# Optimization experiments

Measured on AMD Instinct MI355X. Metric: run time of the kernel, lower is better.

Reference implementation:

```python
import jax, jax.numpy as jnp
import numpy as np

N, D, T = 8192, 512, 12
EPS = 1e-6


def _ln(x, g, b):
    m = jnp.mean(x, axis=-1, keepdims=True)
    v = jnp.mean((x - m) ** 2, axis=-1, keepdims=True)
    return (x - m) / jnp.sqrt(v + EPS) * g + b


def _cross(x1, x2, Wa, ba, Wb, bb, d1, d2):
    # attn_weights2: [N, N], softmax over dim=1 (rows)
    aw2 = jax.nn.softmax((x1 @ Wa.T + ba) @ x2.T, axis=1)
    fused_x2 = (aw2 @ x2) / jnp.sqrt(jnp.float32(d2))
    aw1 = jax.nn.softmax((x2 @ Wb.T + bb) @ x1.T, axis=1)
    fused_x1 = (aw1 @ x1) / jnp.sqrt(jnp.float32(d1))
    return fused_x1, fused_x2


def setup_inputs() -> dict:
    key = jax.random.key(0)
    ks = jax.random.split(key, 16)
    s = 1.0 / np.sqrt(D)
    inp = {
        'xp': jax.random.normal(ks[0], (N, D), jnp.float32),
        'xm': jax.random.normal(ks[1], (N, D), jnp.float32),
        'xs': jax.random.normal(ks[2], (N, D), jnp.float32),
        'ln_g': jnp.ones((D,), jnp.float32),
        'ln_b': jnp.zeros((D,), jnp.float32),
        # mol cross-attention: linear1 (D->D), linear2 (D->D)
        'W1': jax.random.uniform(ks[3], (D, D), jnp.float32, -s, s),
        'b1': jnp.zeros((D,), jnp.float32),
        'W2': jax.random.uniform(ks[4], (D, D), jnp.float32, -s, s),
        'b2': jnp.zeros((D,), jnp.float32),
        # smile cross-attention
        'W3': jax.random.uniform(ks[5], (D, D), jnp.float32, -s, s),
        'b3': jnp.zeros((D,), jnp.float32),
        'W4': jax.random.uniform(ks[6], (D, D), jnp.float32, -s, s),
        'b4': jnp.zeros((D,), jnp.float32),
        # pred head: 2D -> T
        'Wp': jax.random.uniform(ks[7], (T, 2 * D), jnp.float32, -1.0 / np.sqrt(2 * D), 1.0 / np.sqrt(2 * D)),
        'bp': jnp.zeros((T,), jnp.float32),
        # gate
        't': jnp.full((1,), 0.5, jnp.float32),
        'Wt1': jax.random.uniform(ks[8], (50, 1), jnp.float32, -1.0, 1.0),
        'bt1': jnp.zeros((50,), jnp.float32),
        'Wt2': jax.random.uniform(ks[9], (1, 50), jnp.float32, -1.0 / np.sqrt(50), 1.0 / np.sqrt(50)),
        'bt2': jnp.zeros((1,), jnp.float32),
    }
    return inp


def reference(xp, xm, xs, ln_g, ln_b, W1, b1, W2, b2, W3, b3, W4, b4, Wp, bp, t, Wt1, bt1, Wt2, bt2):
    x1 = _ln(xp, ln_g, ln_b)
    x2 = _ln(xm, ln_g, ln_b)
    x3 = x1  # protein encoded twice with same LayerNorm
    x4 = _ln(xs, ln_g, ln_b)

    f1, f2 = _cross(x1, x2, W1, b1, W2, b2, D, D)
    h12 = jnp.concatenate([f1 + x1, f2 + x2], axis=1)          # [N, 2D]
    out12 = jax.nn.relu(h12) @ Wp.T + bp                        # [N, T]

    f3, f4 = _cross(x3, x4, W3, b3, W4, b4, D, D)
    h34 = jnp.concatenate([f3 + x3, f4 + x4], axis=1)
    out34 = jax.nn.relu(h34) @ Wp.T + bp

    t1 = t @ Wt1.T + bt1                                        # [50]
    t2 = jax.nn.sigmoid(t1 @ Wt2.T + bt2)                       # [1]
    return t2 * out12 + (1.0 - t2) * out34
```

## Files before the change

kernel.cpp:

```cpp
#include <hip/hip_runtime.h>
#include <stdint.h>


#define DEV __device__ __forceinline__
typedef unsigned short u16;
typedef __bf16 bf16x8 __attribute__((ext_vector_type(8)));
typedef float f32x4 __attribute__((ext_vector_type(4)));

constexpr int NR = 8192;
constexpr int DDIM = 512;
constexpr int TOUT = 12;

DEV u16 f2b(float f) {
  uint32_t u = __builtin_bit_cast(uint32_t, f);
  u += 0x7fffu + ((u >> 16) & 1u);
  return (u16)(u >> 16);
}
DEV float b2f(u16 h) {
  uint32_t u = ((uint32_t)h) << 16;
  return __builtin_bit_cast(float, u);
}

__global__ __launch_bounds__(256) void prep_kernel(
    const float* __restrict__ xp, const float* __restrict__ xm,
    const float* __restrict__ xs, const float* __restrict__ g,
    const float* __restrict__ b, const float* __restrict__ W1,
    const float* __restrict__ W2, const float* __restrict__ W3,
    const float* __restrict__ W4, u16* __restrict__ o1, u16* __restrict__ o2,
    u16* __restrict__ o4, u16* __restrict__ Wb) {
  int bid = blockIdx.x;
  int tid = threadIdx.x;
  if (bid < 6144) {
    int which = bid >> 11;
    int row = ((bid & 2047) << 2) + (tid >> 6);
    int lane = tid & 63;
    const float* x = which == 0 ? xp : (which == 1 ? xm : xs);
    u16* o = which == 0 ? o1 : (which == 1 ? o2 : o4);
    const float4* xr = (const float4*)(x + (size_t)row * DDIM);
    float4 v0 = xr[lane * 2], v1 = xr[lane * 2 + 1];
    float vals[8] = {v0.x, v0.y, v0.z, v0.w, v1.x, v1.y, v1.z, v1.w};
    float s = 0.f, s2 = 0.f;
    for (int j = 0; j < 8; j++) { s += vals[j]; s2 += vals[j] * vals[j]; }
    for (int off = 1; off < 64; off <<= 1) {
      s += __shfl_xor(s, off);
      s2 += __shfl_xor(s2, off);
    }
    float m = s * (1.0f / DDIM);
    float var = s2 * (1.0f / DDIM) - m * m;
    var = fmaxf(var, 0.f);
    float rs = rsqrtf(var + 1e-6f);
    int d0 = lane * 8;
    u16 us[8];
    for (int j = 0; j < 8; j++)
      us[j] = f2b((vals[j] - m) * rs * g[d0 + j] + b[d0 + j]);
    uint4 pk;
    pk.x = (uint32_t)us[0] | ((uint32_t)us[1] << 16);
    pk.y = (uint32_t)us[2] | ((uint32_t)us[3] << 16);
    pk.z = (uint32_t)us[4] | ((uint32_t)us[5] << 16);
    pk.w = (uint32_t)us[6] | ((uint32_t)us[7] << 16);
    *(uint4*)(o + (size_t)row * DDIM + d0) = pk;
  } else {
    int wbid = bid - 6144;
    int wi = wbid >> 7;
    const float* W = wi == 0 ? W1 : (wi == 1 ? W2 : (wi == 2 ? W3 : W4));
    size_t base = ((size_t)(wbid & 127) * 256 + tid) * 8;
    const float4* src = (const float4*)(W + base);
    float4 a = src[0], c = src[1];
    float vals[8] = {a.x, a.y, a.z, a.w, c.x, c.y, c.z, c.w};
    u16 us[8];
    for (int j = 0; j < 8; j++) us[j] = f2b(vals[j]);
    uint4 pk;
    pk.x = (uint32_t)us[0] | ((uint32_t)us[1] << 16);
    pk.y = (uint32_t)us[2] | ((uint32_t)us[3] << 16);
    pk.z = (uint32_t)us[4] | ((uint32_t)us[5] << 16);
    pk.w = (uint32_t)us[6] | ((uint32_t)us[7] << 16);
    *(uint4*)(Wb + (size_t)wi * DDIM * DDIM + base) = pk;
  }
}

template <int MODE, bool TRIPLE>
DEV void gemm_core(const u16* __restrict__ A, const u16* __restrict__ B,
                   u16* __restrict__ C, const float* __restrict__ bias,
                   u16* lds, int K, int lda, int ldb, int ldc, int bx,
                   int by) {
  constexpr int TM = 4, TN = 4;
  int tid = threadIdx.x;
  int w = tid >> 6, lane = tid & 63;
  int q = lane >> 4, c16 = lane & 15;
  int n0 = bx * 128, m0 = by * 128;
  int wrow = (w >> 1) * 64, wcol = (w & 1) * 64;

  const u16* gptr[4];
  int lof[4];
#pragma unroll
  for (int j = 0; j < 4; j++) {
    int call = w + j * 4;
    bool isA = call < 8;
    int ci = isA ? call : call - 8;
    int chunk = ci * 64 + lane;
    int row = chunk >> 2;
    int gch = ((chunk & 3) - (row >> 1)) & 3;
    gptr[j] = isA ? (A + (size_t)(m0 + row) * lda + gch * 8)
                  : (B + (size_t)(n0 + row) * ldb + gch * 8);
    lof[j] = (isA ? 0 : 4096) + ci * 512;
  }
  auto stageAll = [&](int buf) {
    int bo = buf * 8192;
#pragma unroll
    for (int j = 0; j < 4; j++) {
      __builtin_amdgcn_global_load_lds(
          (const __attribute__((address_space(1))) void*)gptr[j],
          (__attribute__((address_space(3))) void*)(lds + bo + lof[j]), 16, 0,
          0);
      gptr[j] += 32;
    }
  };

  f32x4 acc[TM][TN] = {};
  int nk = K >> 5;
  stageAll(0);
  stageAll(1);
  int cur = 0;
  for (int ks = 0; ks < nk; ks++) {
    if (ks + 1 < nk)
      asm volatile("s_waitcnt vmcnt(4)" ::: "memory");
    else
      asm volatile("s_waitcnt vmcnt(0)" ::: "memory");
    __builtin_amdgcn_sched_barrier(0);
    __builtin_amdgcn_s_barrier();
    __builtin_amdgcn_sched_barrier(0);
    if constexpr (TRIPLE) {
      if (ks + 2 < nk) {
        int nb = cur + 2;
        if (nb >= 3) nb -= 3;
        stageAll(nb);
      }
    }
    const u16* Asm = lds + cur * 8192;
    const u16* Bsm = Asm + 4096;
    bf16x8 af[TM], bfr[TN];
#pragma unroll
    for (int i = 0; i < TM; i++) {
      int r = wrow + i * 16 + c16;
      af[i] = *(const bf16x8*)&Asm[r * 32 + (((q + (r >> 1)) & 3) * 8)];
    }
#pragma unroll
    for (int n = 0; n < TN; n++) {
      int r = wcol + n * 16 + c16;
      bfr[n] = *(const bf16x8*)&Bsm[r * 32 + (((q + (r >> 1)) & 3) * 8)];
    }
    __builtin_amdgcn_s_setprio(1);
#pragma unroll
    for (int i = 0; i < TM; i++)
#pragma unroll
      for (int n = 0; n < TN; n++)
        acc[i][n] = __builtin_amdgcn_mfma_f32_16x16x32_bf16(af[i], bfr[n],
                                                            acc[i][n], 0, 0, 0);
    __builtin_amdgcn_s_setprio(0);
    if constexpr (!TRIPLE) {
      asm volatile("s_waitcnt lgkmcnt(0)" ::: "memory");
      __builtin_amdgcn_sched_barrier(0);
      __builtin_amdgcn_s_barrier();
      __builtin_amdgcn_sched_barrier(0);
      if (ks + 2 < nk) stageAll(cur);
      cur ^= 1;
    } else {
      cur++;
      if (cur >= 3) cur -= 3;
    }
  }
  for (int h = 0; h < 2; h++) {
    __syncthreads();
    if ((w & 1) == h) {
      for (int i = 0; i < TM; i++) {
        for (int n = 0; n < TN; n++) {
          float bv = 0.f;
          if constexpr (MODE == 0) bv = bias[n0 + wcol + n * 16 + c16];
          for (int r = 0; r < 4; r++) {
            int rl = wrow + i * 16 + q * 4 + r;
            int cl = (n * 16 + c16) ^ ((rl & 7) << 3);
            float v = acc[i][n][r];
            if constexpr (MODE == 0) v += bv;
            if constexpr (MODE == 1) v = __expf(v - 48.0f);
            lds[rl * 64 + cl] = f2b(v);
          }
        }
      }
    }
    __syncthreads();
    for (int rep = 0; rep < 4; rep++) {
      int idx = rep * 256 + tid;
      int row = idx >> 3, seg = idx & 7;
      uint4 vv = ((const uint4*)lds)[row * 8 + (seg ^ (row & 7))];
      *(uint4*)(C + (size_t)(m0 + row) * ldc + n0 + h * 64 + seg * 8) = vv;
    }
  }
}

__global__ __launch_bounds__(256, 4) void tqp_kernel(
    const u16* __restrict__ s1, const u16* __restrict__ s2,
    const u16* __restrict__ s4, u16* __restrict__ t1, u16* __restrict__ t2,
    u16* __restrict__ t4, const u16* __restrict__ x1b,
    const u16* __restrict__ Wb, const float* __restrict__ b0,
    u16* __restrict__ Qs) {
  __shared__ u16 lds[16384];
  int bid = blockIdx.x;
  int tid = threadIdx.x;
  if (bid < 256) {
    gemm_core<0, false>(x1b, Wb, Qs, b0, lds, DDIM, DDIM, DDIM, DDIM,
                        bid & 3, bid >> 2);
  } else {
    constexpr int LD = 66;
    u16* tile = lds;
    int tb = bid - 256;
    int which = tb >> 10;
    int rem = tb & 1023;
    int c0 = (rem & 7) * 64;
    int r0 = (rem >> 3) * 64;
    const u16* src = which == 0 ? s1 : (which == 1 ? s2 : s4);
    u16* dst = which == 0 ? t1 : (which == 1 ? t2 : t4);
    for (int c = tid; c < 512; c += 256) {
      int i = c >> 3, j8 = (c & 7) * 8;
      uint4 v = *(const uint4*)(src + (size_t)(r0 + i) * DDIM + c0 + j8);
      uint32_t* dw = (uint32_t*)&tile[i * LD + j8];
      dw[0] = v.x; dw[1] = v.y; dw[2] = v.z; dw[3] = v.w;
    }
    __syncthreads();
    for (int rep = 0; rep < 2; rep++) {
      int idx = rep * 256 + tid;
      int o = idx >> 3, j8 = (idx & 7) * 8;
      u16 us[8];
      for (int k = 0; k < 8; k++) us[k] = tile[(j8 + k) * LD + o];
      uint4 pk;
      pk.x = (uint32_t)us[0] | ((uint32_t)us[1] << 16);
      pk.y = (uint32_t)us[2] | ((uint32_t)us[3] << 16);
      pk.z = (uint32_t)us[4] | ((uint32_t)us[5] << 16);
      pk.w = (uint32_t)us[6] | ((uint32_t)us[7] << 16);
      *(uint4*)(dst + (size_t)(c0 + o) * NR + r0 + j8) = pk;
    }
  }
}

DEV void pv_body(const u16* __restrict__ A, const u16* __restrict__ B,
                 u16* lds, u16* __restrict__ C, int bx, int by) {
  constexpr int BM = 64, BN = 128, BK = 64;
  int tid = threadIdx.x, w = tid >> 6, lane = tid & 63;
  int q = lane >> 4, c16 = lane & 15;
  int n0 = bx * BN, m0 = by * BM;
  int wr = (w >> 1) * 32, wc = (w & 1) * 64;
  f32x4 acc[2][4] = {};
  f32x4 accl[2] = {};
  bf16x8 ones;
  for (int j = 0; j < 8; j++) ones[j] = (__bf16)1.0f;

  const u16* gptr[6];
  int lof0[6], lof1[6];
#pragma unroll
  for (int it = 0; it < 6; it++) {
    int cb = it * 256 + w * 64;
    int c = cb + lane;
    bool isA = cb < 512;
    int ci = isA ? c : c - 512;
    int row = ci >> 3;
    int koff = ((ci & 7) ^ (row & 7)) * 8;
    gptr[it] = isA ? (A + (size_t)(m0 + row) * NR + koff)
                   : (B + (size_t)(n0 + row) * NR + koff);
    lof0[it] = isA ? (cb * 8) : (8192 + (cb - 512) * 8);
    lof1[it] = isA ? (4096 + cb * 8) : (16384 + (cb - 512) * 8);
  }
  auto stage = [&](int buf) {
#pragma unroll
    for (int it = 0; it < 6; it++) {
      int lo = buf ? lof1[it] : lof0[it];
      __builtin_amdgcn_global_load_lds(
          (const __attribute__((address_space(1))) void*)gptr[it],
          (__attribute__((address_space(3))) void*)(lds + lo), 16, 0, 0);
      gptr[it] += BK;
    }
  };

  constexpr int KSTEPS = NR / BK;
  stage(0);
  stage(1);
  for (int ks = 0; ks < KSTEPS; ks++) {
    int cur = ks & 1;
    if (ks + 1 < KSTEPS)
      asm volatile("s_waitcnt vmcnt(6)" ::: "memory");
    else
      asm volatile("s_waitcnt vmcnt(0)" ::: "memory");
    __builtin_amdgcn_sched_barrier(0);
    __builtin_amdgcn_s_barrier();
    __builtin_amdgcn_sched_barrier(0);
    const u16* Asm = lds + cur * 4096;
    const u16* Bsm = lds + 8192 + cur * 8192;
#pragma unroll
    for (int kh = 0; kh < 2; kh++) {
      bf16x8 af[2], bfr[4];
      int cl = kh * 4 + q;
#pragma unroll
      for (int i = 0; i < 2; i++) {
        int r = wr + i * 16 + c16;
        af[i] = *(const bf16x8*)&Asm[r * BK + ((cl ^ (r & 7)) * 8)];
      }
#pragma unroll
      for (int n = 0; n < 4; n++) {
        int r = wc + n * 16 + c16;
        bfr[n] = *(const bf16x8*)&Bsm[r * BK + ((cl ^ (r & 7)) * 8)];
      }
      __builtin_amdgcn_s_setprio(1);
#pragma unroll
      for (int i = 0; i < 2; i++)
        accl[i] = __builtin_amdgcn_mfma_f32_16x16x32_bf16(af[i], ones, accl[i],
                                                          0, 0, 0);
#pragma unroll
      for (int i = 0; i < 2; i++)
#pragma unroll
        for (int n = 0; n < 4; n++)
          acc[i][n] = __builtin_amdgcn_mfma_f32_16x16x32_bf16(
              af[i], bfr[n], acc[i][n], 0, 0, 0);
      __builtin_amdgcn_s_setprio(0);
    }
    asm volatile("s_waitcnt lgkmcnt(0)" ::: "memory");
    __builtin_amdgcn_sched_barrier(0);
    __builtin_amdgcn_s_barrier();
    __builtin_amdgcn_sched_barrier(0);
    if (ks + 2 < KSTEPS) stage(cur);
  }
  for (int i = 0; i < 2; i++) {
    float invl[4];
    for (int r = 0; r < 4; r++)
      invl[r] = 0.044194173824159216f / accl[i][r];
    for (int n = 0; n < 4; n++) {
      int col = n0 + wc + n * 16 + c16;
      for (int r = 0; r < 4; r++) {
        int row = m0 + wr + i * 16 + q * 4 + r;
        C[(size_t)row * DDIM + col] = f2b(acc[i][n][r] * invl[r]);
      }
    }
  }
}

DEV void pv_remap(int bid, int& bx, int& by) {
  bx = (bid >> 3) & 3;
  by = (bid & 7) + 8 * (bid >> 5);
}

__global__ __launch_bounds__(256, 4) void scores_kernel(
    const u16* __restrict__ Q, const u16* __restrict__ Kv,
    u16* __restrict__ P) {
  __shared__ u16 lds[16384];
  gemm_core<1, false>(Q, Kv, P, nullptr, lds, DDIM, DDIM, DDIM, NR,
                      blockIdx.x, blockIdx.y);
}

__global__ __launch_bounds__(256, 4) void qscombo_kernel(
    const u16* __restrict__ x1b, const u16* __restrict__ x2b,
    const u16* __restrict__ x4b, const u16* __restrict__ Wb,
    const float* __restrict__ b1, const float* __restrict__ b2,
    const float* __restrict__ b3, u16* __restrict__ Qs,
    const u16* __restrict__ Q0, u16* __restrict__ P) {
  __shared__ u16 lds[16384];
  if (blockIdx.x < 768) {
    int b = blockIdx.x;
    int z = 1 + (b >> 8), rem = b & 255;
    const u16* A = z == 1 ? x2b : (z == 2 ? x1b : x4b);
    const float* bias = z == 1 ? b1 : (z == 2 ? b2 : b3);
    gemm_core<0, false>(A, Wb + (size_t)z * DDIM * DDIM,
                        Qs + (size_t)z * NR * DDIM, bias, lds, DDIM, DDIM,
                        DDIM, DDIM, rem & 3, rem >> 2);
  } else {
    int b = blockIdx.x - 768;
    gemm_core<1, false>(Q0, x2b, P, nullptr, lds, DDIM, DDIM, DDIM, NR,
                        b & 63, b >> 6);
  }
}

__global__ __launch_bounds__(256, 3) void pv_kernel(
    const u16* __restrict__ A, const u16* __restrict__ B,
    u16* __restrict__ C) {
  __shared__ u16 lds[24576];
  int bx, by;
  pv_remap(blockIdx.x, bx, by);
  pv_body(A, B, lds, C, bx, by);
}

__global__ __launch_bounds__(256, 3) void combo_kernel(
    const u16* __restrict__ Pin, const u16* __restrict__ Vt,
    u16* __restrict__ F, const u16* __restrict__ Q,
    const u16* __restrict__ Kv, u16* __restrict__ Pout) {
  __shared__ u16 lds[24576];
  if (blockIdx.x < 512) {
    int bx, by;
    pv_remap(blockIdx.x, bx, by);
    pv_body(Pin, Vt, lds, F, bx, by);
  } else {
    int b = blockIdx.x - 512;
    gemm_core<1, true>(Q, Kv, Pout, nullptr, lds, DDIM, DDIM, DDIM, NR,
                       b & 63, b >> 6);
  }
}

__global__ __launch_bounds__(256) void head_kernel(
    const u16* __restrict__ F1, const u16* __restrict__ F2,
    const u16* __restrict__ F3, const u16* __restrict__ F4,
    const u16* __restrict__ x1, const u16* __restrict__ x2,
    const u16* __restrict__ x4, const float* __restrict__ Wp,
    const float* __restrict__ bp, const float* __restrict__ tg,
    const float* __restrict__ Wt1, const float* __restrict__ bt1,
    const float* __restrict__ Wt2, const float* __restrict__ bt2,
    float* __restrict__ out) {
  __shared__ float wps[TOUT * 2 * DDIM];
  __shared__ float t2s;
  int tid = threadIdx.x;
  for (int i = tid; i < TOUT * 2 * DDIM; i += 256) wps[i] = Wp[i];
  if (tid == 0) {
    float s = bt2[0];
    for (int k = 0; k < 50; k++) s += Wt2[k] * (tg[0] * Wt1[k] + bt1[k]);
    t2s = 1.0f / (1.0f + __expf(-s));
  }
  __syncthreads();
  int g = tid >> 5, j = tid & 31;
  size_t m = (size_t)blockIdx.x * 8 + g;
  float a12[TOUT] = {}, a34[TOUT] = {};
  for (int d = j; d < 2 * DDIM; d += 32) {
    float h12, h34;
    if (d < DDIM) {
      float xv = b2f(x1[m * DDIM + d]);
      h12 = b2f(F1[m * DDIM + d]) + xv;
      h34 = b2f(F3[m * DDIM + d]) + xv;
    } else {
      int dd = d - DDIM;
      h12 = b2f(F2[m * DDIM + dd]) + b2f(x2[m * DDIM + dd]);
      h34 = b2f(F4[m * DDIM + dd]) + b2f(x4[m * DDIM + dd]);
    }
    h12 = fmaxf(h12, 0.f);
    h34 = fmaxf(h34, 0.f);
    for (int t = 0; t < TOUT; t++) {
      float wv = wps[t * 2 * DDIM + d];
      a12[t] += h12 * wv;
      a34[t] += h34 * wv;
    }
  }
  for (int off = 1; off < 32; off <<= 1)
    for (int t = 0; t < TOUT; t++) {
      a12[t] += __shfl_xor(a12[t], off);
      a34[t] += __shfl_xor(a34[t], off);
    }
  if (j < TOUT) {
    float t2 = t2s;
    out[m * TOUT + j] = t2 * a12[j] + (1.f - t2) * a34[j] + bp[j];
  }
}

extern "C" void kernel_launch(void* const* d_in, const int* in_sizes, int n_in,
                              void* d_out, int out_size, void* d_ws,
                              size_t ws_size, hipStream_t stream) {
  (void)in_sizes; (void)n_in; (void)out_size;
  const float* xp = (const float*)d_in[0];
  const float* xm = (const float*)d_in[1];
  const float* xs = (const float*)d_in[2];
  const float* ln_g = (const float*)d_in[3];
  const float* ln_b = (const float*)d_in[4];
  const float* Wmat[4] = {(const float*)d_in[5], (const float*)d_in[7],
                          (const float*)d_in[9], (const float*)d_in[11]};
  const float* bvec[4] = {(const float*)d_in[6], (const float*)d_in[8],
                          (const float*)d_in[10], (const float*)d_in[12]};
  const float* Wp = (const float*)d_in[13];
  const float* bp = (const float*)d_in[14];
  const float* tg = (const float*)d_in[15];
  const float* Wt1 = (const float*)d_in[16];
  const float* bt1 = (const float*)d_in[17];
  const float* Wt2 = (const float*)d_in[18];
  const float* bt2 = (const float*)d_in[19];
  float* out = (float*)d_out;

  char* ws = (char*)d_ws;
  const size_t MB = 1ull << 20;
  u16* x1b = (u16*)(ws + 0 * MB);
  u16* x2b = (u16*)(ws + 8 * MB);
  u16* x4b = (u16*)(ws + 16 * MB);
  u16* x1t = (u16*)(ws + 24 * MB);
  u16* x2t = (u16*)(ws + 32 * MB);
  u16* x4t = (u16*)(ws + 40 * MB);
  u16* Wb = (u16*)(ws + 48 * MB);
  u16* Qs = (u16*)(ws + 52 * MB);
  u16* P0 = (u16*)(ws + 84 * MB);
  bool dual = ws_size >= 340 * MB;
  u16* P1 = dual ? (u16*)(ws + 212 * MB) : P0;

  prep_kernel<<<dim3(6656), 256, 0, stream>>>(
      xp, xm, xs, ln_g, ln_b, Wmat[0], Wmat[1], Wmat[2], Wmat[3], x1b, x2b,
      x4b, Wb);

  const u16* kvb[4] = {x2b, x1b, x4b, x1b};
  const u16* kvt[4] = {x2t, x1t, x4t, x1t};
  u16* slot[4];
  for (int a = 0; a < 4; a++) slot[a] = Qs + (size_t)a * NR * DDIM;

  tqp_kernel<<<dim3(3328), 256, 0, stream>>>(x1b, x2b, x4b, x1t, x2t, x4t,
                                             x1b, Wb, bvec[0], Qs);

  qscombo_kernel<<<dim3(768 + 64 * 64), 256, 0, stream>>>(
      x1b, x2b, x4b, Wb, bvec[1], bvec[2], bvec[3], Qs, slot[0], P0);

  if (dual) {
    u16* Pb[4] = {P0, P1, P0, P1};
    for (int a = 0; a < 3; a++) {
      combo_kernel<<<dim3(512 + 64 * 64), 256, 0, stream>>>(
          Pb[a], kvt[a], slot[a], slot[a + 1], kvb[a + 1], Pb[a + 1]);
    }
    pv_kernel<<<dim3(512), 256, 0, stream>>>(Pb[3], kvt[3], slot[3]);
  } else {
    for (int a = 0; a < 4; a++) {
      if (a > 0)
        scores_kernel<<<dim3(64, 64), 256, 0, stream>>>(slot[a], kvb[a], P0);
      pv_kernel<<<dim3(512), 256, 0, stream>>>(P0, kvt[a], slot[a]);
    }
  }

  head_kernel<<<dim3(NR / 8), 256, 0, stream>>>(
      slot[1], slot[0], slot[3], slot[2], x1b, x2b, x4b, Wp, bp, tg, Wt1, bt1,
      Wt2, bt2, out);
}
```

Baseline: 868.4 us.

## Split final PV GEMM along K into two halves with a finalize reduction

```diff
diff --git a/kernel.cpp b/kernel.cpp
--- a/kernel.cpp
+++ b/kernel.cpp
@@ -197,7 +197,7 @@
   }
 }
 
-__global__ __launch_bounds__(256, 4) void tqp_kernel(
+__global__ __launch_bounds__(256, 5) void tqp_kernel(
     const u16* __restrict__ s1, const u16* __restrict__ s2,
     const u16* __restrict__ s4, u16* __restrict__ t1, u16* __restrict__ t2,
     u16* __restrict__ t4, const u16* __restrict__ x1b,
@@ -241,8 +241,11 @@
   }
 }
 
+template <bool PARTIAL>
 DEV void pv_body(const u16* __restrict__ A, const u16* __restrict__ B,
-                 u16* lds, u16* __restrict__ C, int bx, int by) {
+                 u16* lds, u16* __restrict__ C, float* __restrict__ Pf,
+                 float* __restrict__ lsum, int kbase, int ksteps, int bx,
+                 int by) {
   constexpr int BM = 64, BN = 128, BK = 64;
   int tid = threadIdx.x, w = tid >> 6, lane = tid & 63;
   int q = lane >> 4, c16 = lane & 15;
@@ -263,8 +266,8 @@
     int ci = isA ? c : c - 512;
     int row = ci >> 3;
     int koff = ((ci & 7) ^ (row & 7)) * 8;
-    gptr[it] = isA ? (A + (size_t)(m0 + row) * NR + koff)
-                   : (B + (size_t)(n0 + row) * NR + koff);
+    gptr[it] = isA ? (A + (size_t)(m0 + row) * NR + kbase + koff)
+                   : (B + (size_t)(n0 + row) * NR + kbase + koff);
     lof0[it] = isA ? (cb * 8) : (8192 + (cb - 512) * 8);
     lof1[it] = isA ? (4096 + cb * 8) : (16384 + (cb - 512) * 8);
   }
@@ -279,12 +282,11 @@
     }
   };
 
-  constexpr int KSTEPS = NR / BK;
   stage(0);
   stage(1);
-  for (int ks = 0; ks < KSTEPS; ks++) {
+  for (int ks = 0; ks < ksteps; ks++) {
     int cur = ks & 1;
-    if (ks + 1 < KSTEPS)
+    if (ks + 1 < ksteps)
       asm volatile("s_waitcnt vmcnt(6)" ::: "memory");
     else
       asm volatile("s_waitcnt vmcnt(0)" ::: "memory");
@@ -324,17 +326,34 @@
     __builtin_amdgcn_sched_barrier(0);
     __builtin_amdgcn_s_barrier();
     __builtin_amdgcn_sched_barrier(0);
-    if (ks + 2 < KSTEPS) stage(cur);
-  }
-  for (int i = 0; i < 2; i++) {
-    float invl[4];
-    for (int r = 0; r < 4; r++)
-      invl[r] = 0.044194173824159216f / accl[i][r];
-    for (int n = 0; n < 4; n++) {
-      int col = n0 + wc + n * 16 + c16;
-      for (int r = 0; r < 4; r++) {
-        int row = m0 + wr + i * 16 + q * 4 + r;
-        C[(size_t)row * DDIM + col] = f2b(acc[i][n][r] * invl[r]);
+    if (ks + 2 < ksteps) stage(cur);
+  }
+  if constexpr (PARTIAL) {
+    for (int i = 0; i < 2; i++) {
+      for (int n = 0; n < 4; n++) {
+        int col = n0 + wc + n * 16 + c16;
+        for (int r = 0; r < 4; r++) {
+          int row = m0 + wr + i * 16 + q * 4 + r;
+          Pf[(size_t)row * DDIM + col] = acc[i][n][r];
+        }
+      }
+    }
+    if ((w & 1) == 0 && c16 == 0) {
+      for (int i = 0; i < 2; i++)
+        for (int r = 0; r < 4; r++)
+          lsum[m0 + wr + i * 16 + q * 4 + r] = accl[i][r];
+    }
+  } else {
+    for (int i = 0; i < 2; i++) {
+      float invl[4];
+      for (int r = 0; r < 4; r++)
+        invl[r] = 0.044194173824159216f / accl[i][r];
+      for (int n = 0; n < 4; n++) {
+        int col = n0 + wc + n * 16 + c16;
+        for (int r = 0; r < 4; r++) {
+          int row = m0 + wr + i * 16 + q * 4 + r;
+          C[(size_t)row * DDIM + col] = f2b(acc[i][n][r] * invl[r]);
+        }
       }
     }
   }
@@ -345,7 +364,7 @@
   by = (bid & 7) + 8 * (bid >> 5);
 }
 
-__global__ __launch_bounds__(256, 4) void scores_kernel(
+__global__ __launch_bounds__(256, 5) void scores_kernel(
     const u16* __restrict__ Q, const u16* __restrict__ Kv,
     u16* __restrict__ P) {
   __shared__ u16 lds[16384];
@@ -353,7 +372,7 @@
                       blockIdx.x, blockIdx.y);
 }
 
-__global__ __launch_bounds__(256, 4) void qscombo_kernel(
+__global__ __launch_bounds__(256, 5) void qscombo_kernel(
     const u16* __restrict__ x1b, const u16* __restrict__ x2b,
     const u16* __restrict__ x4b, const u16* __restrict__ Wb,
     const float* __restrict__ b1, const float* __restrict__ b2,
@@ -381,7 +400,40 @@
   __shared__ u16 lds[24576];
   int bx, by;
   pv_remap(blockIdx.x, bx, by);
-  pv_body(A, B, lds, C, bx, by);
+  pv_body<false>(A, B, lds, C, nullptr, nullptr, 0, 128, bx, by);
+}
+
+__global__ __launch_bounds__(256, 3) void pv_split_kernel(
+    const u16* __restrict__ A, const u16* __restrict__ B,
+    float* __restrict__ Pf, float* __restrict__ ls) {
+  __shared__ u16 lds[24576];
+  int half = blockIdx.x >> 9, inner = blockIdx.x & 511;
+  int bx, by;
+  pv_remap(inner, bx, by);
+  pv_body<true>(A, B, lds, nullptr, Pf + (size_t)half * NR * DDIM,
+                ls + half * NR, half * 4096, 64, bx, by);
+}
+
+__global__ __launch_bounds__(256) void pv_fin_kernel(
+    const float* __restrict__ Pf, const float* __restrict__ ls,
+    u16* __restrict__ F) {
+  int row = blockIdx.x * 4 + (threadIdx.x >> 6);
+  int c0 = (threadIdx.x & 63) * 8;
+  const float* p0 = Pf + (size_t)row * DDIM + c0;
+  const float* p1 = Pf + (size_t)(NR + row) * DDIM + c0;
+  float inv = 0.044194173824159216f / (ls[row] + ls[NR + row]);
+  float4 a0 = *(const float4*)p0, a1 = *(const float4*)(p0 + 4);
+  float4 b0 = *(const float4*)p1, b1 = *(const float4*)(p1 + 4);
+  float v[8] = {a0.x + b0.x, a0.y + b0.y, a0.z + b0.z, a0.w + b0.w,
+                a1.x + b1.x, a1.y + b1.y, a1.z + b1.z, a1.w + b1.w};
+  u16 us[8];
+  for (int j = 0; j < 8; j++) us[j] = f2b(v[j] * inv);
+  uint4 pk;
+  pk.x = (uint32_t)us[0] | ((uint32_t)us[1] << 16);
+  pk.y = (uint32_t)us[2] | ((uint32_t)us[3] << 16);
+  pk.z = (uint32_t)us[4] | ((uint32_t)us[5] << 16);
+  pk.w = (uint32_t)us[6] | ((uint32_t)us[7] << 16);
+  *(uint4*)(F + (size_t)row * DDIM + c0) = pk;
 }
 
 __global__ __launch_bounds__(256, 3) void combo_kernel(
@@ -392,7 +444,7 @@
   if (blockIdx.x < 512) {
     int bx, by;
     pv_remap(blockIdx.x, bx, by);
-    pv_body(Pin, Vt, lds, F, bx, by);
+    pv_body<false>(Pin, Vt, lds, F, nullptr, nullptr, 0, 128, bx, by);
   } else {
     int b = blockIdx.x - 512;
     gemm_core<1, true>(Q, Kv, Pout, nullptr, lds, DDIM, DDIM, DDIM, NR,
@@ -509,7 +561,10 @@
       combo_kernel<<<dim3(512 + 64 * 64), 256, 0, stream>>>(
           Pb[a], kvt[a], slot[a], slot[a + 1], kvb[a + 1], Pb[a + 1]);
     }
-    pv_kernel<<<dim3(512), 256, 0, stream>>>(Pb[3], kvt[3], slot[3]);
+    float* Pf = (float*)P0;
+    float* ls = (float*)(ws + 116 * MB);
+    pv_split_kernel<<<dim3(1024), 256, 0, stream>>>(Pb[3], kvt[3], Pf, ls);
+    pv_fin_kernel<<<dim3(2048), 256, 0, stream>>>(Pf, ls, slot[3]);
   } else {
     for (int a = 0; a < 4; a++) {
       if (a > 0)
```

Result: slower. 2.542 ms (+192.7%).
